# Optimization experiments

Measured on AMD Instinct MI355X. Metric: run time of the kernel, lower is better.

The kernel has to match this reference:

```python
import jax, jax.numpy as jnp
import numpy as np

N_NODES = 25000
N_EDGES = 400000
FEAT = 128
HID = 64
HEADS = 4
NUM_CLASSES = 2
NUM_GRAPHS = 64


def setup_inputs() -> dict:
    key = jax.random.key(0)
    ks = jax.random.split(key, 16)
    x = jax.random.normal(ks[0], (N_NODES, FEAT), dtype=jnp.float32)
    edge_index = jax.random.randint(ks[1], (2, N_EDGES), 0, N_NODES, dtype=jnp.int32)
    batch = jnp.sort(jax.random.randint(ks[2], (N_NODES,), 0, NUM_GRAPHS, dtype=jnp.int32))
    s = 1.0 / np.sqrt(FEAT)
    sh = 1.0 / np.sqrt(HID)
    shc = 1.0 / np.sqrt(HID * HEADS)
    return {
        "x": x,
        "edge_index": edge_index,
        "batch": batch,
        # conv1: GraphConv(FEAT -> HID): lin_rel (bias) on aggregated neighbors + lin_root (no bias)
        "W1_rel": jax.random.uniform(ks[3], (FEAT, HID), jnp.float32, -s, s),
        "b1": jnp.zeros((HID,), jnp.float32),
        "W1_root": jax.random.uniform(ks[4], (FEAT, HID), jnp.float32, -s, s),
        # conv3: GATConv(HID -> HID, heads=HEADS), concat output [N, HEADS*HID]
        "Wg": jax.random.uniform(ks[5], (HID, HEADS * HID), jnp.float32, -sh, sh),
        "att_src": jax.random.uniform(ks[6], (HEADS, HID), jnp.float32, -sh, sh),
        "att_dst": jax.random.uniform(ks[7], (HEADS, HID), jnp.float32, -sh, sh),
        "bg": jnp.zeros((HEADS * HID,), jnp.float32),
        # conv5: GraphConv(HEADS*HID -> HID)
        "W5_rel": jax.random.uniform(ks[8], (HEADS * HID, HID), jnp.float32, -shc, shc),
        "b5": jnp.zeros((HID,), jnp.float32),
        "W5_root": jax.random.uniform(ks[9], (HEADS * HID, HID), jnp.float32, -shc, shc),
        # fc head
        "W_fc1": jax.random.uniform(ks[10], (HID, HID), jnp.float32, -sh, sh),
        "b_fc1": jnp.zeros((HID,), jnp.float32),
        "W_fc2": jax.random.uniform(ks[11], (HID, NUM_CLASSES), jnp.float32, -sh, sh),
        "b_fc2": jnp.zeros((NUM_CLASSES,), jnp.float32),
    }


def _graph_conv(h, src, dst, W_rel, b, W_root):
    # PyG GraphConv (aggr='add'): out_i = W_rel @ sum_{j->i} h_j + b + W_root @ h_i
    agg = jax.ops.segment_sum(h[src], dst, num_segments=N_NODES)
    return agg @ W_rel + b + h @ W_root


def _gat_conv(h, src, dst, Wg, att_src, att_dst, bg):
    # GATConv with default add_self_loops=True; eval mode (no attn dropout)
    n = h.shape[0]
    loop = jnp.arange(n, dtype=src.dtype)
    si = jnp.concatenate([src, loop])
    di = jnp.concatenate([dst, loop])
    xl = (h @ Wg).reshape(n, HEADS, HID)              # [N, H, C]
    a_s = jnp.sum(xl * att_src, axis=-1)              # [N, H]
    a_d = jnp.sum(xl * att_dst, axis=-1)              # [N, H]
    e = jax.nn.leaky_relu(a_s[si] + a_d[di], 0.2)     # [E', H]
    m = jax.ops.segment_max(e, di, num_segments=n)
    p = jnp.exp(e - m[di])
    denom = jax.ops.segment_sum(p, di, num_segments=n)
    alpha = p / denom[di]                             # segment softmax over incoming edges
    out = jax.ops.segment_sum(alpha[:, :, None] * xl[si], di, num_segments=n)
    return out.reshape(n, HEADS * HID) + bg


def reference(x, edge_index, batch, W1_rel, b1, W1_root, Wg, att_src, att_dst, bg,
              W5_rel, b5, W5_root, W_fc1, b_fc1, W_fc2, b_fc2):
    src, dst = edge_index[0], edge_index[1]
    h = jax.nn.relu(_graph_conv(x, src, dst, W1_rel, b1, W1_root))
    h = jax.nn.relu(_gat_conv(h, src, dst, Wg, att_src, att_dst, bg))
    h = jax.nn.relu(_graph_conv(h, src, dst, W5_rel, b5, W5_root))
    g = jax.ops.segment_sum(h, batch, num_segments=NUM_GRAPHS)   # global_add_pool
    g = jax.nn.relu(g @ W_fc1 + b_fc1)
    return jax.nn.sigmoid(g @ W_fc2 + b_fc2)
```

## Files before the change

kernel.cpp:

```cpp
#include <hip/hip_runtime.h>
#include <math.h>

#define N_NODES 25000
#define N_EDGES 400000
#define FEAT 128
#define HID 64
#define HEADS 4
#define HH 256
#define NUM_GRAPHS 64
#define BUCKET 96
#define HS 1601536
#define NPH 25600
#define FILL_BLOCKS 1563

typedef unsigned short ushort_t;
typedef unsigned int uint_t;
typedef __attribute__((ext_vector_type(8))) short short8;
typedef __attribute__((ext_vector_type(4))) float f32x4;

__device__ __forceinline__ float lrelu(float x){ return x > 0.f ? x : 0.2f*x; }

__device__ __forceinline__ ushort_t f2bf(float f){
  uint_t u = __float_as_uint(f);
  return (ushort_t)((u + 0x7fffu + ((u >> 16) & 1u)) >> 16);
}
#define BF_LO(u) __uint_as_float((u) << 16)
#define BF_HI(u) __uint_as_float((u) & 0xffff0000u)

__global__ __launch_bounds__(256) void k_init(
    const float* __restrict__ W1_rel, const float* __restrict__ W1_root,
    const float* __restrict__ W5_rel, const float* __restrict__ W5_root,
    const float* __restrict__ Wg,
    ushort_t* __restrict__ wc1b, ushort_t* __restrict__ wc5b,
    ushort_t* __restrict__ wgb, float* __restrict__ g )
{
  const int e = blockIdx.x*256 + threadIdx.x;
  {
    int j=e&7, lane=(e>>3)&63, kc=(e>>9)&3, nt=e>>11;
    int k = kc*32 + (lane>>4)*8 + j, n = nt*16 + (lane&15);
    float v = (n < 64) ? W1_rel[k*64 + n] : W1_root[k*64 + n - 64];
    wc1b[e] = f2bf(v);
  }
  {
    int j=e&7, lane=(e>>3)&63, kt=(e>>9)&1, nt=e>>10;
    int k = kt*32 + (lane>>4)*8 + j, n = nt*16 + (lane&15);
    wgb[e] = f2bf(Wg[k*HH + n]);
  }
  #pragma unroll
  for (int e5 = e; e5 < 32768; e5 += 16384){
    int j=e5&7, lane=(e5>>3)&63, kc=(e5>>9)&7, nt=e5>>12;
    int k = kc*32 + (lane>>4)*8 + j, n = nt*16 + (lane&15);
    float v = (n < 64) ? W5_rel[k*64 + n] : W5_root[k*64 + n - 64];
    wc5b[e5] = f2bf(v);
  }
  int* z = (int*)g;
  for (int i = e; i < 4096 + N_NODES; i += 16384) z[i] = 0;
}

__global__ __launch_bounds__(256) void k_c1_fill(
    const int* __restrict__ src, const int* __restrict__ dst,
    int* __restrict__ cnt, ushort_t* __restrict__ slot,
    const float* __restrict__ X, const ushort_t* __restrict__ wc1b,
    const float* __restrict__ bias,
    ushort_t* __restrict__ out_rel_b, ushort_t* __restrict__ out_root_b)
{
  if (blockIdx.x < FILL_BLOCKS){
    const int e = blockIdx.x*256 + threadIdx.x;
    if (e < N_EDGES){
      int d = dst[e];
      int pos = atomicAdd(&cnt[d], 1);
      if (pos < BUCKET) slot[(size_t)d*BUCKET + pos] = (ushort_t)src[e];
    }
    return;
  }
  const int wid  = __builtin_amdgcn_readfirstlane(threadIdx.x >> 6);
  const int lane = threadIdx.x & 63;
  const int quad = lane >> 4, col = lane & 15;
  const int nb = (blockIdx.x - FILL_BLOCKS)*64 + wid*16;
  if (nb >= N_NODES) return;
  const int row = min(nb + col, N_NODES-1);
  const float* __restrict__ xr = X + (size_t)row*FEAT + quad*8;
  short8 a[4];
  #pragma unroll
  for (int kc = 0; kc < 4; kc++){
    #pragma unroll
    for (int j = 0; j < 8; j++)
      ((ushort_t*)&a[kc])[j] = f2bf(xr[kc*32 + j]);
  }
  #pragma unroll
  for (int nt = 0; nt < 8; nt++){
    f32x4 d = {0.f,0.f,0.f,0.f};
    #pragma unroll
    for (int kc = 0; kc < 4; kc++){
      short8 b = *(const short8*)(wc1b + ((size_t)(nt*4+kc)*64 + lane)*8);
      d = __builtin_amdgcn_mfma_f32_16x16x32_bf16(a[kc], b, d, 0, 0, 0);
    }
    if (nt < 4){
      #pragma unroll
      for (int r = 0; r < 4; r++){
        const int node = nb + quad*4 + r;
        if (node < N_NODES)
          out_rel_b[(size_t)node*HID + nt*16 + col] = f2bf(d[r]);
      }
    } else {
      const float bv = bias[(nt-4)*16 + col];
      #pragma unroll
      for (int r = 0; r < 4; r++){
        const int node = nb + quad*4 + r;
        if (node < N_NODES)
          out_root_b[(size_t)node*HID + (nt-4)*16 + col] = f2bf(d[r] + bv);
      }
    }
  }
}

__global__ __launch_bounds__(256) void conv5_mfma(
    const ushort_t* __restrict__ h2b_hm, const ushort_t* __restrict__ wc5b,
    const float* __restrict__ bias,
    ushort_t* __restrict__ out_rel_b, ushort_t* __restrict__ out_root_b)
{
  const int wid  = __builtin_amdgcn_readfirstlane(threadIdx.x >> 6);
  const int lane = threadIdx.x & 63;
  const int quad = lane >> 4, col = lane & 15;
  const int nb = blockIdx.x*64 + wid*16;
  if (nb >= N_NODES) return;
  const int row = nb + col;
  short8 a[8];
  #pragma unroll
  for (int kc = 0; kc < 8; kc++){
    const int k0 = kc*32 + quad*8;
    a[kc] = *(const short8*)(h2b_hm + (size_t)(k0>>6)*HS
                             + (size_t)row*HID + (k0&63));
  }
  #pragma unroll
  for (int nt = 0; nt < 8; nt++){
    f32x4 d = {0.f,0.f,0.f,0.f};
    #pragma unroll
    for (int kc = 0; kc < 8; kc++){
      short8 b = *(const short8*)(wc5b + ((size_t)(nt*8+kc)*64 + lane)*8);
      d = __builtin_amdgcn_mfma_f32_16x16x32_bf16(a[kc], b, d, 0, 0, 0);
    }
    if (nt < 4){
      #pragma unroll
      for (int r = 0; r < 4; r++){
        const int node = nb + quad*4 + r;
        if (node < N_NODES)
          out_rel_b[(size_t)node*HID + nt*16 + col] = f2bf(d[r]);
      }
    } else {
      const float bv = bias[(nt-4)*16 + col];
      #pragma unroll
      for (int r = 0; r < 4; r++){
        const int node = nb + quad*4 + r;
        if (node < N_NODES)
          out_root_b[(size_t)node*HID + (nt-4)*16 + col] = f2bf(d[r] + bv);
      }
    }
  }
}

__global__ __launch_bounds__(256) void k3_mfma(
    const ushort_t* __restrict__ h1b, const ushort_t* __restrict__ wgb,
    const float* __restrict__ att_src, const float* __restrict__ att_dst,
    ushort_t* __restrict__ xlb_hm, float* __restrict__ a_s_hm,
    float* __restrict__ a_d_hm)
{
  const int wid  = __builtin_amdgcn_readfirstlane(threadIdx.x >> 6);
  const int lane = threadIdx.x & 63;
  const int quad = lane >> 4, col = lane & 15;
  const int nb = blockIdx.x*64 + wid*16;
  const ushort_t* arow = h1b + (size_t)(nb + col)*HID + quad*8;
  short8 a0 = *(const short8*)(arow);
  short8 a1 = *(const short8*)(arow + 32);
  float as_acc[4] = {0,0,0,0}, ad_acc[4] = {0,0,0,0};
  #pragma unroll
  for (int nt = 0; nt < 16; nt++){
    short8 b0 = *(const short8*)(wgb + ((size_t)(nt*2+0)*64 + lane)*8);
    short8 b1 = *(const short8*)(wgb + ((size_t)(nt*2+1)*64 + lane)*8);
    f32x4 d = {0.f, 0.f, 0.f, 0.f};
    d = __builtin_amdgcn_mfma_f32_16x16x32_bf16(a0, b0, d, 0, 0, 0);
    d = __builtin_amdgcn_mfma_f32_16x16x32_bf16(a1, b1, d, 0, 0, 0);
    const int h = nt >> 2;
    const float asv = att_src[h*HID + (nt & 3)*16 + col];
    const float adv = att_dst[h*HID + (nt & 3)*16 + col];
    #pragma unroll
    for (int r = 0; r < 4; r++){
      const int node = nb + quad*4 + r;
      if (node < N_NODES)
        xlb_hm[(size_t)h*HS + (size_t)node*HID + (nt&3)*16 + col] = f2bf(d[r]);
      as_acc[r] += d[r]*asv;
      ad_acc[r] += d[r]*adv;
    }
    if ((nt & 3) == 3){
      #pragma unroll
      for (int r = 0; r < 4; r++){
        float s1 = as_acc[r], s2 = ad_acc[r];
        #pragma unroll
        for (int off = 1; off < 16; off <<= 1){
          s1 += __shfl_xor(s1, off, 64);
          s2 += __shfl_xor(s2, off, 64);
        }
        const int node = nb + quad*4 + r;
        if (col == 0 && node < N_NODES){
          a_s_hm[h*NPH + node] = s1;
          a_d_hm[h*NPH + node] = s2;
        }
        as_acc[r] = 0.f; ad_acc[r] = 0.f;
      }
    }
  }
}

template<int MODE>
__global__ __launch_bounds__(256) void k_aggb(
    const int* __restrict__ cnt, const ushort_t* __restrict__ slot,
    const ushort_t* __restrict__ featb, const ushort_t* __restrict__ rootb,
    const int* __restrict__ batch, float* __restrict__ g,
    ushort_t* __restrict__ outb)
{
  const int node = blockIdx.x*4 + (threadIdx.x >> 6);
  const int lane = threadIdx.x & 63;
  const ushort_t* __restrict__ sl = slot + (size_t)node*BUCKET;
  const int deg = min(cnt[node], BUCKET);
  const int4 A = ((const int4*)sl)[0];
  const int4 B = ((const int4*)sl)[1];
  const int4 C = ((const int4*)sl)[2];
  const int4 D = ((const int4*)sl)[3];
  const int w[16] = {A.x,A.y,A.z,A.w, B.x,B.y,B.z,B.w,
                     C.x,C.y,C.z,C.w, D.x,D.y,D.z,D.w};
  uint_t uu[32];
  #pragma unroll
  for (int k = 0; k < 32; k++) uu[k] = 0u;
  #pragma unroll
  for (int k = 0; k < 32; k++){
    if (deg > k){
      const int s = (k & 1) ? ((w[k>>1] >> 16) & 0xffff) : (w[k>>1] & 0xffff);
      uu[k] = featb[(size_t)s*HID + lane];
    }
  }
  float acc = BF_LO((uint_t)rootb[(size_t)node*HID + lane]);
  #pragma unroll
  for (int k = 0; k < 32; k++) acc += BF_LO(uu[k]);
  for (int t = 32; t < deg; t++){
    const int s = sl[t];
    acc += BF_LO((uint_t)featb[(size_t)s*HID + lane]);
  }
  const float v = fmaxf(acc, 0.f);
  if (MODE == 0){
    outb[(size_t)node*HID + lane] = f2bf(v);
  } else {
    const int b = batch[node];
    atomicAdd(&g[b*HID + lane], v);
  }
}

__global__ __launch_bounds__(256) void k_gat_node(
    const int* __restrict__ cnt, const ushort_t* __restrict__ slot,
    const ushort_t* __restrict__ xlb_hm, const float* __restrict__ a_s_hm,
    const float* __restrict__ a_d_hm, const float* __restrict__ bg,
    ushort_t* __restrict__ h2b_hm)
{
  const int head = blockIdx.x & 3;
  const int node = (blockIdx.x >> 2)*16 + (threadIdx.x >> 4);
  if (node >= N_NODES) return;
  const int lane = threadIdx.x & 63;
  const int cl = lane & 15;
  const int gb = lane & 48;
  const ushort_t* __restrict__ sl = slot + (size_t)node*BUCKET;
  const int deg = min(cnt[node], BUCKET);
  const ushort_t* __restrict__ xlh = xlb_hm + (size_t)head*HS;
  const float* __restrict__ ash = a_s_hm + head*NPH;
  const float adh = a_d_hm[head*NPH + node];
  float acc0=0, acc1=0, acc2=0, acc3=0;
  float dsum = 0.f;
  for (int base = 0; base < deg; base += 16){
    float pme = 0.f; int sme = node;
    const int e = base + cl;
    if (e < deg){
      sme = sl[e];
      pme = __expf(lrelu(ash[sme] + adh));
    }
    dsum += pme;
    const int nsub = min(16, deg - base);
    int s = 0;
    for (; s + 2 <= nsub; s += 2){
      const float pA = __shfl(pme, gb + s, 64);
      const int   sA = __shfl(sme, gb + s, 64);
      const float pB = __shfl(pme, gb + s + 1, 64);
      const int   sB = __shfl(sme, gb + s + 1, 64);
      uint2 rA = ((const uint2*)(xlh + (size_t)sA*HID))[cl];
      uint2 rB = ((const uint2*)(xlh + (size_t)sB*HID))[cl];
      acc0 += pA*BF_LO(rA.x); acc1 += pA*BF_HI(rA.x);
      acc2 += pA*BF_LO(rA.y); acc3 += pA*BF_HI(rA.y);
      acc0 += pB*BF_LO(rB.x); acc1 += pB*BF_HI(rB.x);
      acc2 += pB*BF_LO(rB.y); acc3 += pB*BF_HI(rB.y);
    }
    if (s < nsub){
      const float pA = __shfl(pme, gb + s, 64);
      const int   sA = __shfl(sme, gb + s, 64);
      uint2 rA = ((const uint2*)(xlh + (size_t)sA*HID))[cl];
      acc0 += pA*BF_LO(rA.x); acc1 += pA*BF_HI(rA.x);
      acc2 += pA*BF_LO(rA.y); acc3 += pA*BF_HI(rA.y);
    }
  }
  #pragma unroll
  for (int off = 1; off < 16; off <<= 1) dsum += __shfl_xor(dsum, off, 64);
  const float pself = __expf(lrelu(ash[node] + adh));
  const float inv = 1.f / (dsum + pself);
  uint2 r = ((const uint2*)(xlh + (size_t)node*HID))[cl];
  acc0 += pself*BF_LO(r.x); acc1 += pself*BF_HI(r.x);
  acc2 += pself*BF_LO(r.y); acc3 += pself*BF_HI(r.y);
  const int col0 = head*HID + cl*4;
  const float ox = fmaxf(acc0*inv + bg[col0+0], 0.f);
  const float oy = fmaxf(acc1*inv + bg[col0+1], 0.f);
  const float oz = fmaxf(acc2*inv + bg[col0+2], 0.f);
  const float ow = fmaxf(acc3*inv + bg[col0+3], 0.f);
  uint2 o;
  o.x = (uint_t)f2bf(ox) | ((uint_t)f2bf(oy) << 16);
  o.y = (uint_t)f2bf(oz) | ((uint_t)f2bf(ow) << 16);
  ((uint2*)(h2b_hm + (size_t)head*HS + (size_t)node*HID))[cl] = o;
}

__global__ __launch_bounds__(256) void k_head(
    const float* __restrict__ g, const float* __restrict__ W1,
    const float* __restrict__ b1, const float* __restrict__ W2,
    const float* __restrict__ b2, float* __restrict__ out)
{
  __shared__ float gs[NUM_GRAPHS*HID];
  __shared__ float hh[NUM_GRAPHS*HID];
  for (int i = threadIdx.x; i < NUM_GRAPHS*HID; i += 256) gs[i] = g[i];
  __syncthreads();
  for (int t = threadIdx.x; t < NUM_GRAPHS*HID; t += 256){
    int b = t >> 6, j = t & 63;
    float acc = b1[j];
    for (int k = 0; k < HID; k++) acc += gs[b*HID+k]*W1[k*HID+j];
    hh[t] = fmaxf(acc, 0.f);
  }
  __syncthreads();
  for (int t = threadIdx.x; t < NUM_GRAPHS*2; t += 256){
    int b = t >> 1, c = t & 1;
    float acc = b2[c];
    for (int k = 0; k < HID; k++) acc += hh[b*HID+k]*W2[k*2+c];
    out[t] = 1.f / (1.f + __expf(-acc));
  }
}

extern "C" void kernel_launch(void* const* d_in, const int* in_sizes, int n_in,
                              void* d_out, int out_size, void* d_ws, size_t ws_size,
                              hipStream_t stream)
{
  const float* x       = (const float*)d_in[0];
  const int*   ei      = (const int*)d_in[1];
  const int*   batch   = (const int*)d_in[2];
  const float* W1_rel  = (const float*)d_in[3];
  const float* b1      = (const float*)d_in[4];
  const float* W1_root = (const float*)d_in[5];
  const float* Wg      = (const float*)d_in[6];
  const float* att_src = (const float*)d_in[7];
  const float* att_dst = (const float*)d_in[8];
  const float* bg      = (const float*)d_in[9];
  const float* W5_rel  = (const float*)d_in[10];
  const float* b5      = (const float*)d_in[11];
  const float* W5_root = (const float*)d_in[12];
  const float* W_fc1   = (const float*)d_in[13];
  const float* b_fc1   = (const float*)d_in[14];
  const float* W_fc2   = (const float*)d_in[15];
  const float* b_fc2   = (const float*)d_in[16];
  const int* src = ei;
  const int* dst = ei + N_EDGES;

  float* ws    = (float*)d_ws;
  ushort_t* xr_b   = (ushort_t*)ws;
  ushort_t* rootb  = (ushort_t*)(ws + 800800);
  ushort_t* h1b    = (ushort_t*)(ws + 2402400);
  ushort_t* xlb_hm = (ushort_t*)(ws + 3203200);
  float*    a_s_hm = ws + 6406304;
  float*    a_d_hm = ws + 6508704;
  ushort_t* h2b_hm = (ushort_t*)(ws + 6611104);
  float*    g      = ws + 9814200;
  int*      cnt    = (int*)(ws + 9818296);
  ushort_t* wc1b   = (ushort_t*)(ws + 9843296);
  ushort_t* wc5b   = (ushort_t*)(ws + 9851488);
  ushort_t* wgb    = (ushort_t*)(ws + 9867872);
  ushort_t* slot   = (ushort_t*)(ws + 9876064);
  float*    out    = (float*)d_out;

  k_init<<<64,256,0,stream>>>(W1_rel, W1_root, W5_rel, W5_root, Wg,
                              wc1b, wc5b, wgb, g);

  k_c1_fill<<<FILL_BLOCKS + (N_NODES+63)/64,256,0,stream>>>(
      src, dst, cnt, slot, x, wc1b, b1, xr_b, rootb);

  k_aggb<0><<<N_NODES/4,256,0,stream>>>(cnt, slot, xr_b, rootb, nullptr, nullptr, h1b);

  k3_mfma<<<(N_NODES+63)/64,256,0,stream>>>(h1b, wgb, att_src, att_dst,
                                            xlb_hm, a_s_hm, a_d_hm);
  k_gat_node<<<((N_NODES+15)/16)*HEADS,256,0,stream>>>(cnt, slot,
      xlb_hm, a_s_hm, a_d_hm, bg, h2b_hm);

  conv5_mfma<<<(N_NODES+63)/64,256,0,stream>>>(h2b_hm, wc5b, b5, xr_b, rootb);
  k_aggb<1><<<N_NODES/4,256,0,stream>>>(cnt, slot, xr_b, rootb, batch, g, nullptr);

  k_head<<<1,256,0,stream>>>(g, W_fc1, b_fc1, W_fc2, b_fc2, out);
}
```

Baseline: 276.4 us.

## Split neighbor aggregation across four wavefronts per node with LDS reduction

The GraphConv aggregation kernel now gives each node a whole 256-thread block instead of a single wavefront. Each of the four waves gathers 8 of the first 32 neighbors, and the last wave also handles any overflow beyond 32. Partial sums are combined through shared memory before the root term, ReLU and output are applied. This cuts per-thread register pressure and the serial gather chain, and exposes more memory-level parallelism. In exchange it launches four times as many blocks, adds a __syncthreads, and wastes loads on padded slots for low-degree nodes.

```diff
diff --git a/kernel.cpp b/kernel.cpp
--- a/kernel.cpp
+++ b/kernel.cpp
@@ -212,45 +212,47 @@
 }
 
 template<int MODE>
-__global__ __launch_bounds__(256) void k_aggb(
+__global__ __launch_bounds__(256, 8) void k_aggb(
     const int* __restrict__ cnt, const ushort_t* __restrict__ slot,
     const ushort_t* __restrict__ featb, const ushort_t* __restrict__ rootb,
     const int* __restrict__ batch, float* __restrict__ g,
     ushort_t* __restrict__ outb)
 {
-  const int node = blockIdx.x*4 + (threadIdx.x >> 6);
+  __shared__ float red[3*HID];
+  const int node = blockIdx.x;
+  const int w    = threadIdx.x >> 6;
   const int lane = threadIdx.x & 63;
   const ushort_t* __restrict__ sl = slot + (size_t)node*BUCKET;
+  const int4 pk = ((const int4*)sl)[w];
+  uint_t rt = 0;
+  if (w == 0) rt = rootb[(size_t)node*HID + lane];
   const int deg = min(cnt[node], BUCKET);
-  const int4 A = ((const int4*)sl)[0];
-  const int4 B = ((const int4*)sl)[1];
-  const int4 C = ((const int4*)sl)[2];
-  const int4 D = ((const int4*)sl)[3];
-  const int w[16] = {A.x,A.y,A.z,A.w, B.x,B.y,B.z,B.w,
-                     C.x,C.y,C.z,C.w, D.x,D.y,D.z,D.w};
-  uint_t uu[32];
-  #pragma unroll
-  for (int k = 0; k < 32; k++) uu[k] = 0u;
-  #pragma unroll
-  for (int k = 0; k < 32; k++){
-    if (deg > k){
-      const int s = (k & 1) ? ((w[k>>1] >> 16) & 0xffff) : (w[k>>1] & 0xffff);
-      uu[k] = featb[(size_t)s*HID + lane];
-    }
-  }
-  float acc = BF_LO((uint_t)rootb[(size_t)node*HID + lane]);
-  #pragma unroll
-  for (int k = 0; k < 32; k++) acc += BF_LO(uu[k]);
-  for (int t = 32; t < deg; t++){
-    const int s = sl[t];
-    acc += BF_LO((uint_t)featb[(size_t)s*HID + lane]);
-  }
-  const float v = fmaxf(acc, 0.f);
-  if (MODE == 0){
-    outb[(size_t)node*HID + lane] = f2bf(v);
-  } else {
-    const int b = batch[node];
-    atomicAdd(&g[b*HID + lane], v);
+  const uint_t pw[4] = {(uint_t)pk.x, (uint_t)pk.y, (uint_t)pk.z, (uint_t)pk.w};
+  uint_t u[8];
+  #pragma unroll
+  for (int j = 0; j < 8; j++){
+    const uint_t s = (j & 1) ? (pw[j>>1] >> 16) : (pw[j>>1] & 0xffffu);
+    u[j] = featb[(size_t)s*HID + lane];
+  }
+  float acc = 0.f;
+  #pragma unroll
+  for (int j = 0; j < 8; j++)
+    acc += (w*8 + j < deg) ? BF_LO(u[j]) : 0.f;
+  if (w == 3)
+    for (int t = 32; t < deg; t++)
+      acc += BF_LO((uint_t)featb[(size_t)sl[t]*HID + lane]);
+  if (w) red[(w-1)*HID + lane] = acc;
+  __syncthreads();
+  if (w == 0){
+    acc += red[lane] + red[HID + lane] + red[2*HID + lane];
+    acc += BF_LO(rt);
+    const float v = fmaxf(acc, 0.f);
+    if (MODE == 0){
+      outb[(size_t)node*HID + lane] = f2bf(v);
+    } else {
+      const int b = batch[node];
+      atomicAdd(&g[b*HID + lane], v);
+    }
   }
 }
 
@@ -391,7 +393,7 @@
   k_c1_fill<<<FILL_BLOCKS + (N_NODES+63)/64,256,0,stream>>>(
       src, dst, cnt, slot, x, wc1b, b1, xr_b, rootb);
 
-  k_aggb<0><<<N_NODES/4,256,0,stream>>>(cnt, slot, xr_b, rootb, nullptr, nullptr, h1b);
+  k_aggb<0><<<N_NODES,256,0,stream>>>(cnt, slot, xr_b, rootb, nullptr, nullptr, h1b);
 
   k3_mfma<<<(N_NODES+63)/64,256,0,stream>>>(h1b, wgb, att_src, att_dst,
                                             xlb_hm, a_s_hm, a_d_hm);
@@ -399,7 +401,7 @@
       xlb_hm, a_s_hm, a_d_hm, bg, h2b_hm);
 
   conv5_mfma<<<(N_NODES+63)/64,256,0,stream>>>(h2b_hm, wc5b, b5, xr_b, rootb);
-  k_aggb<1><<<N_NODES/4,256,0,stream>>>(cnt, slot, xr_b, rootb, batch, g, nullptr);
+  k_aggb<1><<<N_NODES,256,0,stream>>>(cnt, slot, xr_b, rootb, batch, g, nullptr);
 
   k_head<<<1,256,0,stream>>>(g, W_fc1, b_fc1, W_fc2, b_fc2, out);
 }
```

Measured after the change: 255.3 us. 1.08x faster.
